# Kernel tuning notes

Measured on AMD Instinct MI355X. Metric: run time of the kernel, lower is better.

## Reference

```python
import jax, jax.numpy as jnp
import numpy as np
import math

EMBED = 1024
HEADS = 16
HEAD_DIM = EMBED // HEADS
B, S = 2, 2048


def setup_inputs() -> dict:
    key = jax.random.key(0)
    ks = jax.random.split(key, 11)
    s = 1.0 / math.sqrt(EMBED)
    return {
        "query": jax.random.normal(ks[0], (B, S, EMBED), jnp.float32),
        "key_": jax.random.normal(ks[1], (B, S, EMBED), jnp.float32),
        "value": jax.random.normal(ks[2], (B, S, EMBED), jnp.float32),
        "Wq": jax.random.normal(ks[3], (EMBED, EMBED), jnp.float32) * s,
        "bq": jax.random.normal(ks[4], (EMBED,), jnp.float32) * s,
        "Wk": jax.random.normal(ks[5], (EMBED, EMBED), jnp.float32) * s,
        "bk": jax.random.normal(ks[6], (EMBED,), jnp.float32) * s,
        "Wv": jax.random.normal(ks[7], (EMBED, EMBED), jnp.float32) * s,
        "bv": jax.random.normal(ks[8], (EMBED,), jnp.float32) * s,
        "Wo": jax.random.normal(ks[9], (EMBED, EMBED), jnp.float32) * s,
        "bo": jax.random.normal(ks[10], (EMBED,), jnp.float32) * s,
    }


def reference(query, key_, value, Wq, bq, Wk, bk, Wv, bv, Wo, bo):
    b, s, e = query.shape
    # projections (torch Linear: x @ W.T + b)
    q = query @ Wq.T + bq
    k = key_ @ Wk.T + bk
    v = value @ Wv.T + bv
    # [B, H, S, hd]
    q = q.reshape(b, s, HEADS, HEAD_DIM).transpose(0, 2, 1, 3)
    k = k.reshape(b, s, HEADS, HEAD_DIM).transpose(0, 2, 1, 3)
    v = v.reshape(b, s, HEADS, HEAD_DIM).transpose(0, 2, 1, 3)
    scores = jnp.einsum("bhqd,bhkd->bhqk", q, k) / math.sqrt(HEAD_DIM)
    attn = jax.nn.softmax(scores, axis=-1)
    out = jnp.einsum("bhqk,bhkd->bhqd", attn, v)
    out = out.transpose(0, 2, 1, 3).reshape(b, s, e)
    return out @ Wo.T + bo
```

## Files before the change

### kernel.cpp

```cpp
#include <hip/hip_runtime.h>
#include <hip/hip_bf16.h>

using bf16_t = __bf16;
using bf16x4 = __attribute__((ext_vector_type(4))) __bf16;
using bf16x8 = __attribute__((ext_vector_type(8))) __bf16;
using f32x4  = __attribute__((ext_vector_type(4))) float;
using u32 = unsigned int;

constexpr int S_ = 2048, E_ = 1024, M_ = 4096;
constexpr size_t MAT_A = (size_t)M_ * E_;
constexpr size_t MAT_W = (size_t)E_ * E_;

__device__ __forceinline__ bf16_t tobf(float f) {
  unsigned u = __builtin_bit_cast(unsigned, f);
  unsigned short r = (unsigned short)((u + 0x7fffu + ((u >> 16) & 1u)) >> 16);
  return __builtin_bit_cast(bf16_t, r);
}
__device__ __forceinline__ u32 packbf2(float a, float b) {
  u32 ua = __builtin_bit_cast(u32, a) + 0x8000u;
  u32 ub = __builtin_bit_cast(u32, b) + 0x8000u;
  return (ua >> 16) | (ub & 0xffff0000u);
}
__device__ __forceinline__ void async_lds16(const bf16_t* g, bf16_t* l) {
  __builtin_amdgcn_global_load_lds(
      (const __attribute__((address_space(1))) unsigned int*)g,
      (__attribute__((address_space(3))) unsigned int*)l, 16, 0, 0);
}

__global__ __launch_bounds__(256) void cvt_all(
    const float* __restrict__ s0, const float* __restrict__ s1,
    const float* __restrict__ s2, const float* __restrict__ s3,
    const float* __restrict__ s4, const float* __restrict__ s5,
    const float* __restrict__ s6,
    bf16_t* __restrict__ d0, bf16_t* __restrict__ d1,
    bf16_t* __restrict__ d2, bf16_t* __restrict__ d3,
    bf16_t* __restrict__ d4, bf16_t* __restrict__ d5,
    bf16_t* __restrict__ d6) {
  size_t i8 = ((size_t)blockIdx.x * 256 + threadIdx.x) * 8;
  const float* s;
  bf16_t* d;
  size_t off;
  if (i8 < 3 * MAT_A) {
    int w = (int)(i8 >> 22);
    off = i8 & (MAT_A - 1);
    s = w == 0 ? s0 : w == 1 ? s1 : s2;
    d = w == 0 ? d0 : w == 1 ? d1 : d2;
  } else {
    size_t j = i8 - 3 * MAT_A;
    int w = (int)(j >> 20);
    off = j & (MAT_W - 1);
    s = w == 0 ? s3 : w == 1 ? s4 : w == 2 ? s5 : s6;
    d = w == 0 ? d3 : w == 1 ? d4 : w == 2 ? d5 : d6;
  }
  float4 a = *(const float4*)(s + off);
  float4 b = *(const float4*)(s + off + 4);
  bf16x8 o;
  o[0] = tobf(a.x); o[1] = tobf(a.y); o[2] = tobf(a.z); o[3] = tobf(a.w);
  o[4] = tobf(b.x); o[5] = tobf(b.y); o[6] = tobf(b.z); o[7] = tobf(b.w);
  *(bf16x8*)(d + off) = o;
}

__global__ __launch_bounds__(256) void gemm_qkv(
    const bf16_t* __restrict__ xq, const bf16_t* __restrict__ xk,
    const bf16_t* __restrict__ xv, const bf16_t* __restrict__ wq,
    const bf16_t* __restrict__ wk, const bf16_t* __restrict__ wv,
    const float* __restrict__ bq, const float* __restrict__ bk,
    const float* __restrict__ bv, bf16_t* __restrict__ outb,
    bf16_t* __restrict__ Vt) {
  constexpr int K = 1024, N = 1024, BK = 64;
  constexpr float SC = 0.18033688011f;
  __shared__ __align__(16) bf16_t smem[18432];
  bf16_t* As = smem;
  bf16_t* Bs = smem + 128 * BK;

  const int which = blockIdx.y >> 3;
  const bf16_t* X = which == 0 ? xq : which == 1 ? xk : xv;
  const bf16_t* W = which == 0 ? wq : which == 1 ? wk : wv;
  const float* bias = which == 0 ? bq : which == 1 ? bk : bv;
  const int row0 = blockIdx.x * 128, col0 = (blockIdx.y & 7) * 128;

  const int tid = threadIdx.x, lane = tid & 63, wave = tid >> 6;
  const int l15 = lane & 15, q = lane >> 4;
  const int wm = (wave & 1) * 64, wn = (wave >> 1) * 64;
  const f32x4 fzero = {0.f, 0.f, 0.f, 0.f};

  f32x4 acc[4][4];
#pragma unroll
  for (int i = 0; i < 4; ++i)
#pragma unroll
    for (int j = 0; j < 4; ++j) acc[i][j] = fzero;

  const int srow = lane >> 3;
  const int schunk = ((lane & 7) ^ srow) * 8;
  const bf16_t* gA = X + (size_t)(row0 + wave * 32 + srow) * K + schunk;
  const bf16_t* gB = W + (size_t)(col0 + wave * 32 + srow) * K + schunk;
  bf16_t* lA = As + wave * 32 * BK;
  bf16_t* lB = Bs + wave * 32 * BK;

  int ck[2];
  ck[0] = ((q) ^ (l15 & 7)) * 8;
  ck[1] = ((4 + q) ^ (l15 & 7)) * 8;

  for (int k0 = 0; k0 < K; k0 += BK) {
    __syncthreads();
#pragma unroll
    for (int p = 0; p < 4; ++p) {
      async_lds16(gA + k0 + (size_t)(p * 8) * K, lA + p * 8 * BK);
      async_lds16(gB + k0 + (size_t)(p * 8) * K, lB + p * 8 * BK);
    }
    __syncthreads();
#pragma unroll
    for (int h = 0; h < 2; ++h) {
      bf16x8 af[4], bw[4];
#pragma unroll
      for (int i = 0; i < 4; ++i)
        af[i] = *(const bf16x8*)(As + (wm + i * 16 + l15) * BK + ck[h]);
#pragma unroll
      for (int j = 0; j < 4; ++j)
        bw[j] = *(const bf16x8*)(Bs + (wn + j * 16 + l15) * BK + ck[h]);
#pragma unroll
      for (int i = 0; i < 4; ++i)
#pragma unroll
        for (int j = 0; j < 4; ++j)
          acc[i][j] = __builtin_amdgcn_mfma_f32_16x16x32_bf16(af[i], bw[j],
                                                              acc[i][j], 0, 0, 0);
    }
  }

  if (which < 2) {
    const float sc = which == 0 ? SC : 1.0f;
    bf16_t* C = outb + (size_t)which * MAT_A;
#pragma unroll
    for (int j = 0; j < 4; ++j) {
      const int col = col0 + wn + j * 16 + l15;
      const float bc = bias[col];
#pragma unroll
      for (int i = 0; i < 4; ++i)
#pragma unroll
        for (int r = 0; r < 4; ++r) {
          const int row = row0 + wm + i * 16 + q * 4 + r;
          C[(size_t)row * N + col] = tobf((acc[i][j][r] + bc) * sc);
        }
    }
  } else {
    __syncthreads();
    bf16_t* Ep = smem + wave * 4608;
#pragma unroll
    for (int j = 0; j < 4; ++j) {
      const float bc = bias[col0 + wn + j * 16 + l15];
      const int nl = j * 16 + l15;
#pragma unroll
      for (int i = 0; i < 4; ++i) {
        uint2 pk;
        pk.x = packbf2(acc[i][j][0] + bc, acc[i][j][1] + bc);
        pk.y = packbf2(acc[i][j][2] + bc, acc[i][j][3] + bc);
        *(uint2*)(Ep + nl * 72 + i * 16 + q * 4) = pk;
      }
    }
    const int head = (col0 + wn) >> 6;
    const int tok0 = row0 + wm;
    const int bb = tok0 >> 11, tokb = tok0 & 2047;
    const int dl = lane >> 3, ml = (lane & 7) * 8;
#pragma unroll
    for (int p = 0; p < 8; ++p) {
      const int d = dl + p * 8;
      bf16x8 v = *(const bf16x8*)(Ep + d * 72 + ml);
      *(bf16x8*)(Vt + ((size_t)((bb * 16 + head) * 64 + d)) * S_ + tokb + ml) = v;
    }
  }
}

__global__ __launch_bounds__(256) void gemm_o(const bf16_t* __restrict__ X,
                                              const bf16_t* __restrict__ W,
                                              const float* __restrict__ bias,
                                              float* __restrict__ C) {
  constexpr int K = 1024, N = 1024, BK = 64;
  __shared__ __align__(16) bf16_t As[64 * BK];
  __shared__ __align__(16) bf16_t Bs[128 * BK];
  const int tid = threadIdx.x, lane = tid & 63, wave = tid >> 6;
  const int l15 = lane & 15, q = lane >> 4;
  const int row0 = blockIdx.x * 64, col0 = blockIdx.y * 128;
  const int wm = (wave & 1) * 32, wn = (wave >> 1) * 64;
  const f32x4 fzero = {0.f, 0.f, 0.f, 0.f};

  f32x4 acc[2][4];
#pragma unroll
  for (int i = 0; i < 2; ++i)
#pragma unroll
    for (int j = 0; j < 4; ++j) acc[i][j] = fzero;

  const int srow = lane >> 3;
  const int schunk = ((lane & 7) ^ srow) * 8;
  const bf16_t* gA = X + (size_t)(row0 + wave * 16 + srow) * K + schunk;
  const bf16_t* gB = W + (size_t)(col0 + wave * 32 + srow) * K + schunk;
  bf16_t* lA = As + wave * 16 * BK;
  bf16_t* lB = Bs + wave * 32 * BK;

  int ck[2];
  ck[0] = ((q) ^ (l15 & 7)) * 8;
  ck[1] = ((4 + q) ^ (l15 & 7)) * 8;

  for (int k0 = 0; k0 < K; k0 += BK) {
    __syncthreads();
    async_lds16(gA + k0, lA);
    async_lds16(gA + k0 + (size_t)8 * K, lA + 8 * BK);
#pragma unroll
    for (int p = 0; p < 4; ++p)
      async_lds16(gB + k0 + (size_t)(p * 8) * K, lB + p * 8 * BK);
    __syncthreads();
#pragma unroll
    for (int h = 0; h < 2; ++h) {
      bf16x8 af[2], bw[4];
#pragma unroll
      for (int i = 0; i < 2; ++i)
        af[i] = *(const bf16x8*)(As + (wm + i * 16 + l15) * BK + ck[h]);
#pragma unroll
      for (int j = 0; j < 4; ++j)
        bw[j] = *(const bf16x8*)(Bs + (wn + j * 16 + l15) * BK + ck[h]);
#pragma unroll
      for (int i = 0; i < 2; ++i)
#pragma unroll
        for (int j = 0; j < 4; ++j)
          acc[i][j] = __builtin_amdgcn_mfma_f32_16x16x32_bf16(af[i], bw[j],
                                                              acc[i][j], 0, 0, 0);
    }
  }

#pragma unroll
  for (int j = 0; j < 4; ++j) {
    const int col = col0 + wn + j * 16 + l15;
    const float bc = bias[col];
#pragma unroll
    for (int i = 0; i < 2; ++i)
#pragma unroll
      for (int r = 0; r < 4; ++r) {
        const int row = row0 + wm + i * 16 + q * 4 + r;
        C[(size_t)row * N + col] = acc[i][j][r] + bc;
      }
  }
}

__global__ __launch_bounds__(256) void attn_mfma(
    const bf16_t* __restrict__ Qm, const bf16_t* __restrict__ Km,
    const bf16_t* __restrict__ Vtg, bf16_t* __restrict__ Om) {
  constexpr int LDP = 72;
  __shared__ __align__(16) bf16_t Ks[2][64 * 64];
  __shared__ __align__(16) bf16_t Vs[2][64 * 64];
  __shared__ __align__(16) bf16_t Ps[4][2][16 * LDP];

  const int tid = threadIdx.x, lane = tid & 63, wave = tid >> 6;
  const int l15 = lane & 15, q = lane >> 4;
  const int bh = blockIdx.x & 31, qb = blockIdx.x >> 5;
  const int b = bh >> 4, h = bh & 15;
  const size_t rowbase = (size_t)b * S_;
  const int hcol = h * 64;
  const int q0 = qb * 128 + wave * 32;

  const int srow = lane >> 3;
  const int schunk = (lane & 7) ^ srow;
  const bf16_t* gK = Km + (rowbase + wave * 16 + srow) * E_ + hcol + schunk * 8;
  const bf16_t* gV = Vtg + ((size_t)bh * 64 + wave * 16 + srow) * S_ + schunk * 8;

  bf16x8 qf[2][2];
#pragma unroll
  for (int qt = 0; qt < 2; ++qt) {
    const bf16_t* qp = Qm + (rowbase + q0 + qt * 16 + l15) * E_ + hcol + q * 8;
    qf[qt][0] = *(const bf16x8*)qp;
    qf[qt][1] = *(const bf16x8*)(qp + 32);
  }

  bf16x8 onesv;
#pragma unroll
  for (int j = 0; j < 8; ++j)
    onesv[j] = __builtin_bit_cast(bf16_t, (unsigned short)0x3F80);

  const f32x4 fzero = {0.f, 0.f, 0.f, 0.f};
  f32x4 oacc[2][4];
#pragma unroll
  for (int qt = 0; qt < 2; ++qt)
#pragma unroll
    for (int mt = 0; mt < 4; ++mt) oacc[qt][mt] = fzero;
  f32x4 lsacc[2] = {fzero, fzero};

  const int rbase = l15 * 64;
  int ck[2];
  ck[0] = ((q) ^ (l15 & 7)) * 8;
  ck[1] = ((4 + q) ^ (l15 & 7)) * 8;
  bf16_t* pw0 = Ps[wave][0] + l15 * LDP;
  bf16_t* pw1 = Ps[wave][1] + l15 * LDP;

  async_lds16(gK, Ks[0] + wave * 1024);
  async_lds16(gK + (size_t)8 * E_, Ks[0] + wave * 1024 + 512);
  async_lds16(gV, Vs[0] + wave * 1024);
  async_lds16(gV + (size_t)8 * S_, Vs[0] + wave * 1024 + 512);

  for (int t = 0; t < 32; ++t) {
    const int pb = t & 1;
    __syncthreads();
    if (t + 1 < 32) {
      const size_t koff = (size_t)((t + 1) * 64) * E_;
      const int voff = (t + 1) * 64;
      bf16_t* dK = Ks[pb ^ 1] + wave * 1024;
      bf16_t* dV = Vs[pb ^ 1] + wave * 1024;
      async_lds16(gK + koff, dK);
      async_lds16(gK + koff + (size_t)8 * E_, dK + 512);
      async_lds16(gV + voff, dV);
      async_lds16(gV + voff + (size_t)8 * S_, dV + 512);
    }
    const bf16_t* Kbuf = Ks[pb];
    const bf16_t* Vbuf = Vs[pb];

#pragma unroll
    for (int nt = 0; nt < 4; ++nt) {
      bf16x8 a0 = *(const bf16x8*)(Kbuf + nt * 1024 + rbase + ck[0]);
      bf16x8 a1 = *(const bf16x8*)(Kbuf + nt * 1024 + rbase + ck[1]);
#pragma unroll
      for (int qt = 0; qt < 2; ++qt) {
        f32x4 st = fzero;
        st = __builtin_amdgcn_mfma_f32_16x16x32_bf16(a0, qf[qt][0], st, 0, 0, 0);
        st = __builtin_amdgcn_mfma_f32_16x16x32_bf16(a1, qf[qt][1], st, 0, 0, 0);
        uint2 pk;
        pk.x = packbf2(__builtin_amdgcn_exp2f(st[0]), __builtin_amdgcn_exp2f(st[1]));
        pk.y = packbf2(__builtin_amdgcn_exp2f(st[2]), __builtin_amdgcn_exp2f(st[3]));
        *(uint2*)((qt ? pw1 : pw0) + nt * 16 + q * 4) = pk;
      }
    }

#pragma unroll
    for (int kk = 0; kk < 2; ++kk) {
      bf16x8 bp0 = *(const bf16x8*)(pw0 + kk * 32 + q * 8);
      bf16x8 bp1 = *(const bf16x8*)(pw1 + kk * 32 + q * 8);
      lsacc[0] = __builtin_amdgcn_mfma_f32_16x16x32_bf16(onesv, bp0, lsacc[0], 0, 0, 0);
      lsacc[1] = __builtin_amdgcn_mfma_f32_16x16x32_bf16(onesv, bp1, lsacc[1], 0, 0, 0);
#pragma unroll
      for (int mt = 0; mt < 4; ++mt) {
        bf16x8 av = *(const bf16x8*)(Vbuf + mt * 1024 + rbase + ck[kk]);
        oacc[0][mt] = __builtin_amdgcn_mfma_f32_16x16x32_bf16(av, bp0,
                                                              oacc[0][mt], 0, 0, 0);
        oacc[1][mt] = __builtin_amdgcn_mfma_f32_16x16x32_bf16(av, bp1,
                                                              oacc[1][mt], 0, 0, 0);
      }
    }
  }

#pragma unroll
  for (int qt = 0; qt < 2; ++qt) {
    const float inv = 1.0f / lsacc[qt][0];
    const size_t orow = (rowbase + q0 + qt * 16 + l15) * E_ + hcol + q * 4;
#pragma unroll
    for (int mt = 0; mt < 4; ++mt) {
      bf16x4 o;
#pragma unroll
      for (int r = 0; r < 4; ++r) o[r] = tobf(oacc[qt][mt][r] * inv);
      *(bf16x4*)(Om + orow + mt * 16) = o;
    }
  }
}

extern "C" void kernel_launch(void* const* d_in, const int* in_sizes, int n_in,
                              void* d_out, int out_size, void* d_ws, size_t ws_size,
                              hipStream_t stream) {
  const float* query = (const float*)d_in[0];
  const float* key_  = (const float*)d_in[1];
  const float* value = (const float*)d_in[2];
  const float* Wq = (const float*)d_in[3];
  const float* bq = (const float*)d_in[4];
  const float* Wk = (const float*)d_in[5];
  const float* bk = (const float*)d_in[6];
  const float* Wv = (const float*)d_in[7];
  const float* bv = (const float*)d_in[8];
  const float* Wo = (const float*)d_in[9];
  const float* bo = (const float*)d_in[10];

  bf16_t* qc  = (bf16_t*)d_ws;
  bf16_t* kc  = qc + MAT_A;
  bf16_t* vc  = kc + MAT_A;
  bf16_t* wqb = vc + MAT_A;
  bf16_t* wkb = wqb + MAT_W;
  bf16_t* wvb = wkb + MAT_W;
  bf16_t* wob = wvb + MAT_W;
  bf16_t* Qb  = wob + MAT_W;
  bf16_t* Kb  = Qb + MAT_A;
  bf16_t* Vt  = Kb + MAT_A;
  bf16_t* AOb = Vt + MAT_A;

  cvt_all<<<8192, 256, 0, stream>>>(query, key_, value, Wq, Wk, Wv, Wo,
                                    qc, kc, vc, wqb, wkb, wvb, wob);
  gemm_qkv<<<dim3(32, 24), 256, 0, stream>>>(qc, kc, vc, wqb, wkb, wvb,
                                             bq, bk, bv, Qb, Vt);
  attn_mfma<<<512, 256, 0, stream>>>(Qb, Kb, Vt, AOb);
  gemm_o<<<dim3(64, 8), 256, 0, stream>>>(AOb, wob, bo, (float*)d_out);
}
```

Before: 223.0 us.

## Keep softmax probabilities in registers via permlane swaps, halve attention tile

The attention kernel no longer stages the exponentiated scores through shared memory. It uses permlane32/permlane16 swaps to rearrange the packed bf16 values from the score MFMA output layout into the operand layout of the PV MFMA, which removes an LDS write/read round trip per tile. Each wave now handles 16 query rows instead of 32, so the grid doubles to 1024 blocks and occupancy hints (launch_bounds 4) and s_setprio around the PV MFMAs are added. The cost is that each K/V tile loaded into LDS is reused by half as many queries, so global and LDS traffic per FLOP goes up.

New measurement: 215.5 us. 3.4% less time.

```diff
diff --git a/kernel.cpp b/kernel.cpp
--- a/kernel.cpp
+++ b/kernel.cpp
@@ -2,10 +2,13 @@
 #include <hip/hip_bf16.h>
 
 using bf16_t = __bf16;
+using bf16x2 = __attribute__((ext_vector_type(2))) __bf16;
 using bf16x4 = __attribute__((ext_vector_type(4))) __bf16;
 using bf16x8 = __attribute__((ext_vector_type(8))) __bf16;
 using f32x4  = __attribute__((ext_vector_type(4))) float;
 using u32 = unsigned int;
+using u32x4 = __attribute__((ext_vector_type(4))) u32;
+using i32x2 = __attribute__((ext_vector_type(2))) int;
 
 constexpr int S_ = 2048, E_ = 1024, M_ = 4096;
 constexpr size_t MAT_A = (size_t)M_ * E_;
@@ -20,6 +23,22 @@
   u32 ua = __builtin_bit_cast(u32, a) + 0x8000u;
   u32 ub = __builtin_bit_cast(u32, b) + 0x8000u;
   return (ua >> 16) | (ub & 0xffff0000u);
+}
+__device__ __forceinline__ u32 cvtpk(float lo, float hi) {
+  bf16x2 t;
+  t[0] = (bf16_t)lo;
+  t[1] = (bf16_t)hi;
+  return __builtin_bit_cast(u32, t);
+}
+__device__ __forceinline__ void swap32(u32& a, u32& b) {
+  i32x2 r = __builtin_amdgcn_permlane32_swap((int)a, (int)b, false, false);
+  a = (u32)r[0];
+  b = (u32)r[1];
+}
+__device__ __forceinline__ void swap16(u32& a, u32& b) {
+  i32x2 r = __builtin_amdgcn_permlane16_swap((int)a, (int)b, false, false);
+  a = (u32)r[0];
+  b = (u32)r[1];
 }
 __device__ __forceinline__ void async_lds16(const bf16_t* g, bf16_t* l) {
   __builtin_amdgcn_global_load_lds(
@@ -240,13 +259,11 @@
   }
 }
 
-__global__ __launch_bounds__(256) void attn_mfma(
+__global__ __launch_bounds__(256, 4) void attn_mfma(
     const bf16_t* __restrict__ Qm, const bf16_t* __restrict__ Km,
     const bf16_t* __restrict__ Vtg, bf16_t* __restrict__ Om) {
-  constexpr int LDP = 72;
   __shared__ __align__(16) bf16_t Ks[2][64 * 64];
   __shared__ __align__(16) bf16_t Vs[2][64 * 64];
-  __shared__ __align__(16) bf16_t Ps[4][2][16 * LDP];
 
   const int tid = threadIdx.x, lane = tid & 63, wave = tid >> 6;
   const int l15 = lane & 15, q = lane >> 4;
@@ -254,19 +271,18 @@
   const int b = bh >> 4, h = bh & 15;
   const size_t rowbase = (size_t)b * S_;
   const int hcol = h * 64;
-  const int q0 = qb * 128 + wave * 32;
+  const int q0 = qb * 64 + wave * 16;
 
   const int srow = lane >> 3;
   const int schunk = (lane & 7) ^ srow;
   const bf16_t* gK = Km + (rowbase + wave * 16 + srow) * E_ + hcol + schunk * 8;
   const bf16_t* gV = Vtg + ((size_t)bh * 64 + wave * 16 + srow) * S_ + schunk * 8;
 
-  bf16x8 qf[2][2];
-#pragma unroll
-  for (int qt = 0; qt < 2; ++qt) {
-    const bf16_t* qp = Qm + (rowbase + q0 + qt * 16 + l15) * E_ + hcol + q * 8;
-    qf[qt][0] = *(const bf16x8*)qp;
-    qf[qt][1] = *(const bf16x8*)(qp + 32);
+  bf16x8 qf[2];
+  {
+    const bf16_t* qp = Qm + (rowbase + q0 + l15) * E_ + hcol + q * 8;
+    qf[0] = *(const bf16x8*)qp;
+    qf[1] = *(const bf16x8*)(qp + 32);
   }
 
   bf16x8 onesv;
@@ -275,19 +291,15 @@
     onesv[j] = __builtin_bit_cast(bf16_t, (unsigned short)0x3F80);
 
   const f32x4 fzero = {0.f, 0.f, 0.f, 0.f};
-  f32x4 oacc[2][4];
-#pragma unroll
-  for (int qt = 0; qt < 2; ++qt)
-#pragma unroll
-    for (int mt = 0; mt < 4; ++mt) oacc[qt][mt] = fzero;
-  f32x4 lsacc[2] = {fzero, fzero};
+  f32x4 oacc[4];
+#pragma unroll
+  for (int mt = 0; mt < 4; ++mt) oacc[mt] = fzero;
+  f32x4 lsacc = fzero;
 
   const int rbase = l15 * 64;
   int ck[2];
   ck[0] = ((q) ^ (l15 & 7)) * 8;
   ck[1] = ((4 + q) ^ (l15 & 7)) * 8;
-  bf16_t* pw0 = Ps[wave][0] + l15 * LDP;
-  bf16_t* pw1 = Ps[wave][1] + l15 * LDP;
 
   async_lds16(gK, Ks[0] + wave * 1024);
   async_lds16(gK + (size_t)8 * E_, Ks[0] + wave * 1024 + 512);
@@ -310,50 +322,45 @@
     const bf16_t* Kbuf = Ks[pb];
     const bf16_t* Vbuf = Vs[pb];
 
+    u32 uu[4][2];
 #pragma unroll
     for (int nt = 0; nt < 4; ++nt) {
       bf16x8 a0 = *(const bf16x8*)(Kbuf + nt * 1024 + rbase + ck[0]);
       bf16x8 a1 = *(const bf16x8*)(Kbuf + nt * 1024 + rbase + ck[1]);
-#pragma unroll
-      for (int qt = 0; qt < 2; ++qt) {
-        f32x4 st = fzero;
-        st = __builtin_amdgcn_mfma_f32_16x16x32_bf16(a0, qf[qt][0], st, 0, 0, 0);
-        st = __builtin_amdgcn_mfma_f32_16x16x32_bf16(a1, qf[qt][1], st, 0, 0, 0);
-        uint2 pk;
-        pk.x = packbf2(__builtin_amdgcn_exp2f(st[0]), __builtin_amdgcn_exp2f(st[1]));
-        pk.y = packbf2(__builtin_amdgcn_exp2f(st[2]), __builtin_amdgcn_exp2f(st[3]));
-        *(uint2*)((qt ? pw1 : pw0) + nt * 16 + q * 4) = pk;
-      }
+      f32x4 st = fzero;
+      st = __builtin_amdgcn_mfma_f32_16x16x32_bf16(a0, qf[0], st, 0, 0, 0);
+      st = __builtin_amdgcn_mfma_f32_16x16x32_bf16(a1, qf[1], st, 0, 0, 0);
+      uu[nt][0] = cvtpk(__builtin_amdgcn_exp2f(st[0]), __builtin_amdgcn_exp2f(st[1]));
+      uu[nt][1] = cvtpk(__builtin_amdgcn_exp2f(st[2]), __builtin_amdgcn_exp2f(st[3]));
     }
 
 #pragma unroll
     for (int kk = 0; kk < 2; ++kk) {
-      bf16x8 bp0 = *(const bf16x8*)(pw0 + kk * 32 + q * 8);
-      bf16x8 bp1 = *(const bf16x8*)(pw1 + kk * 32 + q * 8);
-      lsacc[0] = __builtin_amdgcn_mfma_f32_16x16x32_bf16(onesv, bp0, lsacc[0], 0, 0, 0);
-      lsacc[1] = __builtin_amdgcn_mfma_f32_16x16x32_bf16(onesv, bp1, lsacc[1], 0, 0, 0);
+      u32 A = uu[2 * kk][0], Bv = uu[2 * kk][1];
+      u32 C = uu[2 * kk + 1][0], D = uu[2 * kk + 1][1];
+      swap32(A, C);  swap16(A, C);
+      swap32(Bv, D); swap16(Bv, D);
+      u32x4 w = {A, Bv, C, D};
+      bf16x8 bp = __builtin_bit_cast(bf16x8, w);
+      lsacc = __builtin_amdgcn_mfma_f32_16x16x32_bf16(onesv, bp, lsacc, 0, 0, 0);
+      __builtin_amdgcn_s_setprio(1);
 #pragma unroll
       for (int mt = 0; mt < 4; ++mt) {
         bf16x8 av = *(const bf16x8*)(Vbuf + mt * 1024 + rbase + ck[kk]);
-        oacc[0][mt] = __builtin_amdgcn_mfma_f32_16x16x32_bf16(av, bp0,
-                                                              oacc[0][mt], 0, 0, 0);
-        oacc[1][mt] = __builtin_amdgcn_mfma_f32_16x16x32_bf16(av, bp1,
-                                                              oacc[1][mt], 0, 0, 0);
+        oacc[mt] = __builtin_amdgcn_mfma_f32_16x16x32_bf16(av, bp, oacc[mt], 0, 0, 0);
       }
-    }
-  }
-
-#pragma unroll
-  for (int qt = 0; qt < 2; ++qt) {
-    const float inv = 1.0f / lsacc[qt][0];
-    const size_t orow = (rowbase + q0 + qt * 16 + l15) * E_ + hcol + q * 4;
-#pragma unroll
-    for (int mt = 0; mt < 4; ++mt) {
-      bf16x4 o;
-#pragma unroll
-      for (int r = 0; r < 4; ++r) o[r] = tobf(oacc[qt][mt][r] * inv);
-      *(bf16x4*)(Om + orow + mt * 16) = o;
-    }
+      __builtin_amdgcn_s_setprio(0);
+    }
+  }
+
+  const float inv = 1.0f / lsacc[0];
+  const size_t orow = (rowbase + q0 + l15) * E_ + hcol + q * 4;
+#pragma unroll
+  for (int mt = 0; mt < 4; ++mt) {
+    bf16x4 o;
+#pragma unroll
+    for (int r = 0; r < 4; ++r) o[r] = tobf(oacc[mt][r] * inv);
+    *(bf16x4*)(Om + orow + mt * 16) = o;
   }
 }
 
@@ -388,6 +395,6 @@
                                     qc, kc, vc, wqb, wkb, wvb, wob);
   gemm_qkv<<<dim3(32, 24), 256, 0, stream>>>(qc, kc, vc, wqb, wkb, wvb,
                                              bq, bk, bv, Qb, Vt);
-  attn_mfma<<<512, 256, 0, stream>>>(Qb, Kb, Vt, AOb);
+  attn_mfma<<<1024, 256, 0, stream>>>(Qb, Kb, Vt, AOb);
   gemm_o<<<dim3(64, 8), 256, 0, stream>>>(AOb, wob, bo, (float*)d_out);
 }
```

## Keep attention P tile in registers via permlane swaps instead of LDS

Applied to the files above, without the earlier changes.

The attention kernel no longer writes the exponentiated score tile P to shared memory and reads it back in the B-operand layout. It packs P into bf16 pairs with the native convert and rearranges them across lanes using permlane32/permlane16 swaps, so the PV MFMAs consume P straight from registers. This removes per-wave LDS traffic and a store-to-load round trip, and frees shared memory. It also adds launch bounds of 2 blocks per CU and raises wave priority around the PV MFMA block, at the cost of more register pressure and new cross-lane instructions.

New measurement: 210.8 us. 5.5% less time.

```diff
diff --git a/kernel.cpp b/kernel.cpp
--- a/kernel.cpp
+++ b/kernel.cpp
@@ -2,10 +2,13 @@
 #include <hip/hip_bf16.h>
 
 using bf16_t = __bf16;
+using bf16x2 = __attribute__((ext_vector_type(2))) __bf16;
 using bf16x4 = __attribute__((ext_vector_type(4))) __bf16;
 using bf16x8 = __attribute__((ext_vector_type(8))) __bf16;
 using f32x4  = __attribute__((ext_vector_type(4))) float;
 using u32 = unsigned int;
+using u32x4 = __attribute__((ext_vector_type(4))) u32;
+using i32x2 = __attribute__((ext_vector_type(2))) int;
 
 constexpr int S_ = 2048, E_ = 1024, M_ = 4096;
 constexpr size_t MAT_A = (size_t)M_ * E_;
@@ -20,6 +23,22 @@
   u32 ua = __builtin_bit_cast(u32, a) + 0x8000u;
   u32 ub = __builtin_bit_cast(u32, b) + 0x8000u;
   return (ua >> 16) | (ub & 0xffff0000u);
+}
+__device__ __forceinline__ u32 cvtpk(float lo, float hi) {
+  bf16x2 t;
+  t[0] = (bf16_t)lo;
+  t[1] = (bf16_t)hi;
+  return __builtin_bit_cast(u32, t);
+}
+__device__ __forceinline__ void swap32(u32& a, u32& b) {
+  i32x2 r = __builtin_amdgcn_permlane32_swap((int)a, (int)b, false, false);
+  a = (u32)r[0];
+  b = (u32)r[1];
+}
+__device__ __forceinline__ void swap16(u32& a, u32& b) {
+  i32x2 r = __builtin_amdgcn_permlane16_swap((int)a, (int)b, false, false);
+  a = (u32)r[0];
+  b = (u32)r[1];
 }
 __device__ __forceinline__ void async_lds16(const bf16_t* g, bf16_t* l) {
   __builtin_amdgcn_global_load_lds(
@@ -240,13 +259,11 @@
   }
 }
 
-__global__ __launch_bounds__(256) void attn_mfma(
+__global__ __launch_bounds__(256, 2) void attn_mfma(
     const bf16_t* __restrict__ Qm, const bf16_t* __restrict__ Km,
     const bf16_t* __restrict__ Vtg, bf16_t* __restrict__ Om) {
-  constexpr int LDP = 72;
   __shared__ __align__(16) bf16_t Ks[2][64 * 64];
   __shared__ __align__(16) bf16_t Vs[2][64 * 64];
-  __shared__ __align__(16) bf16_t Ps[4][2][16 * LDP];
 
   const int tid = threadIdx.x, lane = tid & 63, wave = tid >> 6;
   const int l15 = lane & 15, q = lane >> 4;
@@ -286,8 +303,6 @@
   int ck[2];
   ck[0] = ((q) ^ (l15 & 7)) * 8;
   ck[1] = ((4 + q) ^ (l15 & 7)) * 8;
-  bf16_t* pw0 = Ps[wave][0] + l15 * LDP;
-  bf16_t* pw1 = Ps[wave][1] + l15 * LDP;
 
   async_lds16(gK, Ks[0] + wave * 1024);
   async_lds16(gK + (size_t)8 * E_, Ks[0] + wave * 1024 + 512);
@@ -310,6 +325,7 @@
     const bf16_t* Kbuf = Ks[pb];
     const bf16_t* Vbuf = Vs[pb];
 
+    u32 uu[2][4][2];
 #pragma unroll
     for (int nt = 0; nt < 4; ++nt) {
       bf16x8 a0 = *(const bf16x8*)(Kbuf + nt * 1024 + rbase + ck[0]);
@@ -319,27 +335,37 @@
         f32x4 st = fzero;
         st = __builtin_amdgcn_mfma_f32_16x16x32_bf16(a0, qf[qt][0], st, 0, 0, 0);
         st = __builtin_amdgcn_mfma_f32_16x16x32_bf16(a1, qf[qt][1], st, 0, 0, 0);
-        uint2 pk;
-        pk.x = packbf2(__builtin_amdgcn_exp2f(st[0]), __builtin_amdgcn_exp2f(st[1]));
-        pk.y = packbf2(__builtin_amdgcn_exp2f(st[2]), __builtin_amdgcn_exp2f(st[3]));
-        *(uint2*)((qt ? pw1 : pw0) + nt * 16 + q * 4) = pk;
+        uu[qt][nt][0] =
+            cvtpk(__builtin_amdgcn_exp2f(st[0]), __builtin_amdgcn_exp2f(st[1]));
+        uu[qt][nt][1] =
+            cvtpk(__builtin_amdgcn_exp2f(st[2]), __builtin_amdgcn_exp2f(st[3]));
       }
     }
 
 #pragma unroll
     for (int kk = 0; kk < 2; ++kk) {
-      bf16x8 bp0 = *(const bf16x8*)(pw0 + kk * 32 + q * 8);
-      bf16x8 bp1 = *(const bf16x8*)(pw1 + kk * 32 + q * 8);
-      lsacc[0] = __builtin_amdgcn_mfma_f32_16x16x32_bf16(onesv, bp0, lsacc[0], 0, 0, 0);
-      lsacc[1] = __builtin_amdgcn_mfma_f32_16x16x32_bf16(onesv, bp1, lsacc[1], 0, 0, 0);
+      bf16x8 bp[2];
+#pragma unroll
+      for (int qt = 0; qt < 2; ++qt) {
+        u32 A = uu[qt][2 * kk][0], Bv = uu[qt][2 * kk][1];
+        u32 C = uu[qt][2 * kk + 1][0], D = uu[qt][2 * kk + 1][1];
+        swap32(A, C);  swap16(A, C);
+        swap32(Bv, D); swap16(Bv, D);
+        u32x4 w = {A, Bv, C, D};
+        bp[qt] = __builtin_bit_cast(bf16x8, w);
+        lsacc[qt] =
+            __builtin_amdgcn_mfma_f32_16x16x32_bf16(onesv, bp[qt], lsacc[qt], 0, 0, 0);
+      }
+      __builtin_amdgcn_s_setprio(1);
 #pragma unroll
       for (int mt = 0; mt < 4; ++mt) {
         bf16x8 av = *(const bf16x8*)(Vbuf + mt * 1024 + rbase + ck[kk]);
-        oacc[0][mt] = __builtin_amdgcn_mfma_f32_16x16x32_bf16(av, bp0,
-                                                              oacc[0][mt], 0, 0, 0);
-        oacc[1][mt] = __builtin_amdgcn_mfma_f32_16x16x32_bf16(av, bp1,
-                                                              oacc[1][mt], 0, 0, 0);
+        oacc[0][mt] =
+            __builtin_amdgcn_mfma_f32_16x16x32_bf16(av, bp[0], oacc[0][mt], 0, 0, 0);
+        oacc[1][mt] =
+            __builtin_amdgcn_mfma_f32_16x16x32_bf16(av, bp[1], oacc[1][mt], 0, 0, 0);
       }
+      __builtin_amdgcn_s_setprio(0);
     }
   }
 
```
